# Kernel optimization log

Measured on AMD Instinct MI355X. Metric: run time of the kernel, lower is better.

## Reference

```python
import jax, jax.numpy as jnp
import numpy as np

FEAT_STRIDE = 16
ANCHOR_SCALES = (8.0, 16.0, 32.0)
ANCHOR_RATIOS = (0.5, 1.0, 2.0)
PRE_NMS_TOPN = 12000
POST_NMS_TOPN = 2000
NMS_THRESH = 0.7
MIN_SIZE = 16.0


def _mkanchors(ws, hs, cx, cy):
    return np.stack([cx - 0.5 * (ws - 1), cy - 0.5 * (hs - 1),
                     cx + 0.5 * (ws - 1), cy + 0.5 * (hs - 1)], axis=1)


def generate_anchors(base_size=16, ratios=ANCHOR_RATIOS, scales=ANCHOR_SCALES):
    ratios = np.asarray(ratios, np.float32)
    scales = np.asarray(scales, np.float32)
    w = h = float(base_size)
    cx = cy = 0.5 * (base_size - 1)
    size = w * h
    ws = np.round(np.sqrt(size / ratios))
    hs = np.round(ws * ratios)
    ratio_anchors = _mkanchors(ws, hs, cx, cy)
    out = []
    for a in ratio_anchors:
        aw = a[2] - a[0] + 1.0
        ah = a[3] - a[1] + 1.0
        acx = a[0] + 0.5 * (aw - 1)
        acy = a[1] + 0.5 * (ah - 1)
        out.append(_mkanchors(aw * scales, ah * scales, acx, acy))
    return np.concatenate(out, axis=0).astype(np.float32)  # (A, 4)


ANCHORS = generate_anchors(FEAT_STRIDE)
NUM_ANCHORS = ANCHORS.shape[0]  # 9


def _proposal_forward(scores, bbox_deltas, im_info):
    A = NUM_ANCHORS
    fg = scores[:, A:, :, :]                       # (1, A, H, W) foreground scores
    H, W = fg.shape[-2], fg.shape[-1]
    im_h, im_w, im_scale = im_info[0, 0], im_info[0, 1], im_info[0, 2]

    # anchor grid
    sx = jnp.arange(W, dtype=jnp.float32) * FEAT_STRIDE
    sy = jnp.arange(H, dtype=jnp.float32) * FEAT_STRIDE
    gy, gx = jnp.meshgrid(sy, sx, indexing='ij')
    shifts = jnp.stack([gx.ravel(), gy.ravel(), gx.ravel(), gy.ravel()], axis=1)  # (K,4)
    anchors = jnp.asarray(ANCHORS)[None, :, :] + shifts[:, None, :]
    anchors = anchors.reshape(-1, 4)               # (K*A, 4)

    deltas = jnp.transpose(bbox_deltas, (0, 2, 3, 1)).reshape(-1, 4)
    sc = jnp.transpose(fg, (0, 2, 3, 1)).reshape(-1)

    # bbox_transform_inv
    aw = anchors[:, 2] - anchors[:, 0] + 1.0
    ah = anchors[:, 3] - anchors[:, 1] + 1.0
    acx = anchors[:, 0] + 0.5 * aw
    acy = anchors[:, 1] + 0.5 * ah
    pcx = deltas[:, 0] * aw + acx
    pcy = deltas[:, 1] * ah + acy
    pw = jnp.exp(deltas[:, 2]) * aw
    ph = jnp.exp(deltas[:, 3]) * ah
    x1 = pcx - 0.5 * pw
    y1 = pcy - 0.5 * ph
    x2 = pcx + 0.5 * pw
    y2 = pcy + 0.5 * ph

    # clip_boxes (scale slot in the clip call is 1.0 in the original)
    x1 = jnp.clip(x1, 0.0, im_w - 1.0)
    x2 = jnp.clip(x2, 0.0, im_w - 1.0)
    y1 = jnp.clip(y1, 0.0, im_h - 1.0)
    y2 = jnp.clip(y2, 0.0, im_h - 1.0)
    props = jnp.stack([x1, y1, x2, y2], axis=1)

    # _filter_boxes: mask instead of gather (jit-safe fixed shapes)
    ms = MIN_SIZE * im_scale
    valid = ((x2 - x1 + 1.0) >= ms) & ((y2 - y1 + 1.0) >= ms)
    sc_m = jnp.where(valid, sc, -jnp.inf)

    # descending sort + pre-NMS top-k in one shot
    top_sc, order = jax.lax.top_k(sc_m, PRE_NMS_TOPN)
    p = props[order]                               # (preN, 4) sorted by score desc
    vk = valid[order]

    pn = jax.lax.stop_gradient(p)
    areas = (pn[:, 2] - pn[:, 0] + 1.0) * (pn[:, 3] - pn[:, 1] + 1.0)
    xx1 = jnp.maximum(pn[:, 0][:, None], pn[:, 0][None, :])
    yy1 = jnp.maximum(pn[:, 1][:, None], pn[:, 1][None, :])
    xx2 = jnp.minimum(pn[:, 2][:, None], pn[:, 2][None, :])
    yy2 = jnp.minimum(pn[:, 3][:, None], pn[:, 3][None, :])
    inter = jnp.maximum(xx2 - xx1 + 1.0, 0.0) * jnp.maximum(yy2 - yy1 + 1.0, 0.0)
    iou = inter / (areas[:, None] + areas[None, :] - inter)
    sup_mat = iou > NMS_THRESH                     # (preN, preN) bool

    idx = jnp.arange(PRE_NMS_TOPN, dtype=jnp.int32)

    def body(keep, xs):
        sup_row, i = xs
        keep = jnp.where(keep[i], keep & ~(sup_row & (idx > i)), keep)
        return keep, None

    keep, _ = jax.lax.scan(body, vk, (sup_mat, idx))

    # keep[:post_nms_topN] with fixed shapes: rank kept boxes, scatter into slots
    rank = jnp.cumsum(keep.astype(jnp.int32)) - 1
    slot_src = jnp.where(keep & (rank < POST_NMS_TOPN), rank, POST_NMS_TOPN)
    slots = jnp.full((POST_NMS_TOPN,), PRE_NMS_TOPN, jnp.int32).at[slot_src].set(idx, mode='drop')

    p_pad = jnp.concatenate([p, jnp.zeros((1, 4), p.dtype)], axis=0)
    s_pad = jnp.concatenate([top_sc, jnp.zeros((1,), top_sc.dtype)], axis=0)
    boxes = p_pad[slots]
    out_sc = s_pad[slots][:, None]
    rois = jnp.concatenate([jnp.zeros((POST_NMS_TOPN, 1), boxes.dtype), boxes], axis=1)
    return rois, out_sc


def setup_inputs() -> dict:
    key = jax.random.key(0)
    k1, k2 = jax.random.split(key)
    H = W = 512
    scores = jax.random.normal(k1, (1, 2 * NUM_ANCHORS, H, W), jnp.float32)
    bbox_deltas = jax.random.normal(k2, (1, 4 * NUM_ANCHORS, H, W), jnp.float32) * 0.2
    im_info = jnp.array([[float(H * FEAT_STRIDE), float(W * FEAT_STRIDE), 1.0]], jnp.float32)
    return {"scores": scores, "bbox_deltas": bbox_deltas, "im_info": im_info}


def reference(scores, bbox_deltas, im_info):
    return _proposal_forward(scores, bbox_deltas, im_info)
```

## Files before the change

### kernel.cpp

```cpp
#include <hip/hip_runtime.h>
#include <hip/hip_bf16.h>
#include <stdint.h>

#pragma clang fp contract(off)

#define FH 512
#define FW 512
#define NA 9
#define HW (FH*FW)
#define TOTAL (HW*NA)
#define PRE_NMS 12000
#define POST_NMS 2000
#define NMS_WORDS 188
#define MROW 192
#define CAND_MAX 16384
#define NMS_TH 0.7f
#define MIN_SIZE_C 16.0f

__constant__ float ANCH[NA][4] = {
  {-84.f,-40.f,99.f,55.f},
  {-176.f,-88.f,191.f,103.f},
  {-360.f,-184.f,375.f,199.f},
  {-56.f,-56.f,71.f,71.f},
  {-120.f,-120.f,135.f,135.f},
  {-248.f,-248.f,263.f,263.f},
  {-36.f,-80.f,51.f,95.f},
  {-80.f,-168.f,95.f,183.f},
  {-168.f,-344.f,183.f,359.f}
};

__device__ __forceinline__ void decode_box(int a, int h, int w,
    const float* __restrict__ deltas, float im_h, float im_w,
    float& x1, float& y1, float& x2, float& y2) {
  float sx = (float)(w * 16);
  float sy = (float)(h * 16);
  float ax1 = ANCH[a][0] + sx;
  float ay1 = ANCH[a][1] + sy;
  float ax2 = ANCH[a][2] + sx;
  float ay2 = ANCH[a][3] + sy;
  float aw = ax2 - ax1 + 1.0f;
  float ah = ay2 - ay1 + 1.0f;
  float acx = ax1 + 0.5f * aw;
  float acy = ay1 + 0.5f * ah;
  int base = h * FW + w;
  float d0 = deltas[(4*a+0)*HW + base];
  float d1 = deltas[(4*a+1)*HW + base];
  float d2 = deltas[(4*a+2)*HW + base];
  float d3 = deltas[(4*a+3)*HW + base];
  float pcx = d0 * aw + acx;
  float pcy = d1 * ah + acy;
  float pw = expf(d2) * aw;
  float ph = expf(d3) * ah;
  x1 = pcx - 0.5f * pw;
  y1 = pcy - 0.5f * ph;
  x2 = pcx + 0.5f * pw;
  y2 = pcy + 0.5f * ph;
  x1 = fminf(fmaxf(x1, 0.0f), im_w - 1.0f);
  x2 = fminf(fmaxf(x2, 0.0f), im_w - 1.0f);
  y1 = fminf(fmaxf(y1, 0.0f), im_h - 1.0f);
  y2 = fminf(fmaxf(y2, 0.0f), im_h - 1.0f);
}

__global__ void k_keys(const float* __restrict__ scores, const float* __restrict__ deltas,
                       const float* __restrict__ im_info, unsigned* __restrict__ keys,
                       unsigned* __restrict__ hist8) {
  __shared__ unsigned lh[256];
  int t = threadIdx.x;
  lh[t] = 0;
  __syncthreads();
  int base = blockIdx.x * blockDim.x + t;
  float im_h = im_info[0], im_w = im_info[1];
  float ms = MIN_SIZE_C * im_info[2];
  int h = base / FW, w = base % FW;
  for (int a = 0; a < NA; a++) {
    float x1, y1, x2, y2;
    decode_box(a, h, w, deltas, im_h, im_w, x1, y1, x2, y2);
    bool valid = ((x2 - x1 + 1.0f) >= ms) && ((y2 - y1 + 1.0f) >= ms);
    float sc = scores[(NA + a)*HW + base];
    float v = valid ? sc : -INFINITY;
    unsigned u = __float_as_uint(v);
    unsigned mono = (u & 0x80000000u) ? ~u : (u | 0x80000000u);
    keys[base*NA + a] = mono;
    atomicAdd(&lh[mono >> 24], 1u);
  }
  __syncthreads();
  atomicAdd(&hist8[t], lh[t]);
}

__global__ void __launch_bounds__(256) k_refine15(const unsigned* __restrict__ keys,
    const unsigned* __restrict__ hist8, unsigned* __restrict__ hist15) {
  __shared__ unsigned ssum[256];
  __shared__ unsigned sB8;
  int t = threadIdx.x;
  unsigned hv = hist8[t];
  ssum[t] = hv;
  __syncthreads();
  for (int off = 1; off < 256; off <<= 1) {
    unsigned v = ssum[t];
    unsigned add = (t + off < 256) ? ssum[t + off] : 0u;
    __syncthreads();
    ssum[t] = v + add;
    __syncthreads();
  }
  unsigned above = ssum[t] - hv;
  if (above < PRE_NMS && above + hv >= PRE_NMS) sB8 = (unsigned)t;
  __syncthreads();
  unsigned B8 = sB8;
  int stride = gridDim.x * blockDim.x;
  for (int i = blockIdx.x * blockDim.x + t; i < TOTAL; i += stride) {
    unsigned k = keys[i];
    if ((k >> 24) == B8) atomicAdd(&hist15[(k >> 9) & 0x7FFFu], 1u);
  }
}

__global__ void __launch_bounds__(256) k_compact(const unsigned* __restrict__ keys,
    const unsigned* __restrict__ hist8, const unsigned* __restrict__ hist15,
    unsigned* __restrict__ cnt, unsigned long long* __restrict__ cand) {
  __shared__ unsigned ssum[256];
  __shared__ unsigned sB8, sT2, sB15;
  int t = threadIdx.x;
  unsigned hv = hist8[t];
  ssum[t] = hv;
  __syncthreads();
  for (int off = 1; off < 256; off <<= 1) {
    unsigned v = ssum[t];
    unsigned add = (t + off < 256) ? ssum[t + off] : 0u;
    __syncthreads();
    ssum[t] = v + add;
    __syncthreads();
  }
  unsigned above = ssum[t] - hv;
  if (above < PRE_NMS && above + hv >= PRE_NMS) { sB8 = (unsigned)t; sT2 = PRE_NMS - above; }
  __syncthreads();
  unsigned B8 = sB8, T2 = sT2;
  unsigned loc = 0;
  for (int i = 0; i < 128; i++) loc += hist15[t*128 + i];
  __syncthreads();
  ssum[t] = loc;
  __syncthreads();
  for (int off = 1; off < 256; off <<= 1) {
    unsigned v = ssum[t];
    unsigned add = (t + off < 256) ? ssum[t + off] : 0u;
    __syncthreads();
    ssum[t] = v + add;
    __syncthreads();
  }
  unsigned above15 = ssum[t] - loc;
  unsigned acc = above15;
  for (int i = 127; i >= 0; i--) {
    unsigned cb = hist15[t*128 + i];
    acc += cb;
    if (acc >= T2 && acc - cb < T2) sB15 = (unsigned)(t*128 + i);
  }
  __syncthreads();
  unsigned K = (B8 << 24) | (sB15 << 9);
  int stride = gridDim.x * blockDim.x;
  for (int i = blockIdx.x * blockDim.x + t; i < TOTAL; i += stride) {
    unsigned k = keys[i];
    if (k >= K) {
      unsigned pos = atomicAdd(cnt, 1u);
      if (pos < CAND_MAX)
        cand[pos] = ((unsigned long long)k << 32) | (unsigned)(~(unsigned)i);
    }
  }
}

__global__ void __launch_bounds__(256) k_rank(const unsigned* __restrict__ pcnt,
    const unsigned long long* __restrict__ cand,
    const float* __restrict__ deltas, const float* __restrict__ im_info,
    float4* __restrict__ boxes, float* __restrict__ scoresArr,
    unsigned long long* __restrict__ remvInit) {
  __shared__ unsigned long long tile[2048];
  unsigned cnt = *pcnt;
  if (cnt > CAND_MAX) cnt = CAND_MAX;
  int i = blockIdx.x * 256 + threadIdx.x;
  unsigned long long mine = (i < (int)cnt) ? cand[i] : 0ULL;
  int rank = 0;
  for (unsigned t0 = 0; t0 < cnt; t0 += 2048) {
    unsigned n = min(2048u, cnt - t0);
    __syncthreads();
    for (unsigned j = threadIdx.x; j < n; j += 256) tile[j] = cand[t0 + j];
    __syncthreads();
    if (i < (int)cnt) {
      int q0 = 0, q1 = 0, q2 = 0, q3 = 0;
      unsigned j = 0;
      #pragma unroll 4
      for (; j + 4 <= n; j += 4) {
        q0 += (tile[j]   > mine) ? 1 : 0;
        q1 += (tile[j+1] > mine) ? 1 : 0;
        q2 += (tile[j+2] > mine) ? 1 : 0;
        q3 += (tile[j+3] > mine) ? 1 : 0;
      }
      for (; j < n; j++) q0 += (tile[j] > mine) ? 1 : 0;
      rank += q0 + q1 + q2 + q3;
    }
  }
  if (i < (int)cnt && rank < PRE_NMS) {
    unsigned mono = (unsigned)(mine >> 32);
    unsigned idx = ~(unsigned)(mine & 0xFFFFFFFFull);
    unsigned u = (mono & 0x80000000u) ? (mono ^ 0x80000000u) : ~mono;
    float sc = __uint_as_float(u);
    int a = idx % NA;
    int base = idx / NA;
    int h = base / FW, w = base % FW;
    float x1, y1, x2, y2;
    decode_box(a, h, w, deltas, im_info[0], im_info[1], x1, y1, x2, y2);
    boxes[rank] = make_float4(x1, y1, x2, y2);
    scoresArr[rank] = sc;
    if (sc > -INFINITY)
      atomicAnd(&remvInit[rank >> 6], ~(1ULL << (rank & 63)));
  }
}

__global__ void __launch_bounds__(64) k_mask(const float4* __restrict__ boxes,
                                             unsigned long long* __restrict__ mask) {
  int wg = blockIdx.x;
  int bi = blockIdx.y;
  if (wg * 8 + 7 < bi) return;
  __shared__ float4 jb[8][64];
  int t = threadIdx.x;
  #pragma unroll
  for (int k = 0; k < 8; k++) {
    int jg = (wg * 8 + k) * 64 + t;
    jb[k][t] = (jg < PRE_NMS) ? boxes[jg] : make_float4(0.f, 0.f, -1.f, -1.f);
  }
  __syncthreads();
  int i = bi * 64 + t;
  if (i >= PRE_NMS) return;
  float4 b = boxes[i];
  float area_i = (b.z - b.x + 1.0f) * (b.w - b.y + 1.0f);
  unsigned long long bits[8];
  #pragma unroll
  for (int k = 0; k < 8; k++) {
    unsigned long long bb = 0;
    for (int jj = 0; jj < 64; jj++) {
      float4 o = jb[k][jj];
      float xx1 = fmaxf(b.x, o.x);
      float yy1 = fmaxf(b.y, o.y);
      float xx2 = fminf(b.z, o.z);
      float yy2 = fminf(b.w, o.w);
      float iw = fmaxf(xx2 - xx1 + 1.0f, 0.0f);
      float ih = fmaxf(yy2 - yy1 + 1.0f, 0.0f);
      float inter = iw * ih;
      float area_o = (o.z - o.x + 1.0f) * (o.w - o.y + 1.0f);
      float iou = inter / (area_i + area_o - inter);
      if (iou > NMS_TH) bb |= (1ULL << jj);
    }
    bits[k] = bb;
  }
  size_t rb = (size_t)i * MROW + wg * 8;
  #pragma unroll
  for (int k = 0; k < 8; k++) mask[rb + k] = bits[k];
}

__global__ void __launch_bounds__(64) k_nms(const unsigned long long* __restrict__ mask,
    const unsigned long long* __restrict__ remvI,
    const float4* __restrict__ boxes, const float* __restrict__ scoresArr,
    float* __restrict__ out) {
  extern __shared__ unsigned long long dyn[];
  unsigned long long* stage = dyn;
  unsigned* klist = (unsigned*)(dyn + 64 * MROW);
  int lane = threadIdx.x;
  unsigned long long r0 = remvI[lane];
  unsigned long long r1 = remvI[64 + lane];
  unsigned long long r2 = remvI[128 + lane];
  unsigned long long W = __shfl(r0, 0);
  unsigned long long diagc = mask[(size_t)lane * MROW + 0];
  unsigned long long nw1c  = mask[(size_t)lane * MROW + 1];
  int kept_cnt = 0, nkPrev = 0;
  bool done = false;
  for (int c = 0; c < NMS_WORDS; c++) {
    bool more = (c + 1 < NMS_WORDS);
    unsigned long long diagN = 0, nw1N = 0;
    if (more) {
      size_t rb = (size_t)((c + 1) * 64 + lane) * MROW;
      diagN = mask[rb + (c + 1)];
      if (c + 2 < NMS_WORDS) nw1N = mask[rb + (c + 2)];
    }
    int gi0 = c * 64;
    int jmax = PRE_NMS - gi0; if (jmax > 64) jmax = 64;
    unsigned long long avail = ~W;
    if (jmax < 64) avail &= ((1ULL << jmax) - 1ULL);
    unsigned long long keptmask = 0;
    while (avail) {
      int j = __ffsll((long long)avail) - 1;
      keptmask |= (1ULL << j);
      if (lane == 0) klist[kept_cnt] = (unsigned)(gi0 + j);
      kept_cnt++;
      if (kept_cnt >= POST_NMS) { done = true; break; }
      unsigned long long supp = __shfl(diagc, j);
      avail &= ~supp;
      avail &= ~((2ULL << j) - 1ULL);
    }
    if (done || !more) break;
    unsigned long long A = ((keptmask >> lane) & 1ULL) ? nw1c : 0ULL;
    asm volatile("s_waitcnt vmcnt(0)" ::: "memory");
    __builtin_amdgcn_sched_barrier(0);
    for (int s = 0; s < nkPrev; s++) {
      r0 |= stage[s * MROW + lane];
      r1 |= stage[s * MROW + 64 + lane];
      r2 |= stage[s * MROW + 128 + lane];
    }
    unsigned long long x = A;
    #pragma unroll
    for (int off = 32; off; off >>= 1) x |= __shfl_xor(x, off);
    int cw = c + 1;
    unsigned long long Rw = ((cw >> 6) == 0) ? r0 : (((cw >> 6) == 1) ? r1 : r2);
    W = __shfl(Rw, cw & 63) | x;
    int slot = 0;
    unsigned long long km = keptmask;
    while (km) {
      int j = __ffsll((long long)km) - 1; km &= km - 1;
      const char* rb = (const char*)(mask + (size_t)(gi0 + j) * MROW);
      char* lb = (char*)(void*)stage + slot * 1536;
      __builtin_amdgcn_global_load_lds(
          (const __attribute__((address_space(1))) unsigned*)(rb + lane * 16),
          (__attribute__((address_space(3))) unsigned*)lb, 16, 0, 0);
      if (lane < 30)
        __builtin_amdgcn_global_load_lds(
            (const __attribute__((address_space(1))) unsigned*)(rb + 1024 + lane * 16),
            (__attribute__((address_space(3))) unsigned*)(lb + 1024), 16, 0, 0);
      slot++;
    }
    nkPrev = slot;
    diagc = diagN; nw1c = nw1N;
  }
  __syncthreads();
  for (int s = lane; s < POST_NMS; s += 64) {
    float x1 = 0.f, y1 = 0.f, x2 = 0.f, y2 = 0.f, sc = 0.f;
    if (s < kept_cnt) {
      unsigned r = klist[s];
      float4 b = boxes[r];
      x1 = b.x; y1 = b.y; x2 = b.z; y2 = b.w;
      sc = scoresArr[r];
    }
    out[s*5 + 0] = 0.f;
    out[s*5 + 1] = x1;
    out[s*5 + 2] = y1;
    out[s*5 + 3] = x2;
    out[s*5 + 4] = y2;
    out[POST_NMS*5 + s] = sc;
  }
}

extern "C" void kernel_launch(void* const* d_in, const int* in_sizes, int n_in,
                              void* d_out, int out_size, void* d_ws, size_t ws_size,
                              hipStream_t stream) {
  const float* scores  = (const float*)d_in[0];
  const float* deltas  = (const float*)d_in[1];
  const float* im_info = (const float*)d_in[2];
  float* out = (float*)d_out;
  char* ws = (char*)d_ws;

  unsigned* keys             = (unsigned*)(ws + 0);
  unsigned* hist8            = (unsigned*)(ws + 9437184);
  unsigned* hist15           = (unsigned*)(ws + 9438208);
  unsigned* scal             = (unsigned*)(ws + 9569280);
  unsigned long long* remvI  = (unsigned long long*)(ws + 9569536);
  unsigned long long* cand   = (unsigned long long*)(ws + 9571072);
  float4* boxes              = (float4*)(ws + 9702144);
  float* scoresArr           = (float*)(ws + 9894144);
  unsigned long long* mask   = (unsigned long long*)(ws + 9942144);

  hipMemsetAsync(ws + 9437184, 0, 132352, stream);
  hipMemsetAsync(ws + 9569536, 0xFF, 1536, stream);

  k_keys<<<HW/256, 256, 0, stream>>>(scores, deltas, im_info, keys, hist8);
  k_refine15<<<256, 256, 0, stream>>>(keys, hist8, hist15);
  k_compact<<<256, 256, 0, stream>>>(keys, hist8, hist15, &scal[4], cand);
  k_rank<<<CAND_MAX/256, 256, 0, stream>>>(&scal[4], cand, deltas, im_info,
                                           boxes, scoresArr, remvI);
  dim3 mg(24, 188);
  k_mask<<<mg, 64, 0, stream>>>(boxes, mask);

  (void)hipFuncSetAttribute((const void*)k_nms,
        hipFuncAttributeMaxDynamicSharedMemorySize, 64*MROW*8 + 2000*4);
  k_nms<<<1, 64, 64*MROW*8 + 2000*4, stream>>>(mask, remvI, boxes, scoresArr, out);
}
```

Measured before the change: 1.012 ms.

## Fuse proposal stages into one cooperative kernel and tighten NMS scan

Replaces the two memsets and five separate kernels (keys, refine, compact, rank, mask) with one cooperative persistent kernel that uses grid syncs between phases. The key layout becomes anchor-major for coalesced stores, and ranking is split across 8 blocks per candidate group with atomic partial sums. In the NMS kernel, shuffles become readlanes, suppression words are accumulated inside the keep loop, and mask rows are prefetched two chunks ahead. This removes launch and memset overhead at the cost of grid-wide barriers and fixed 512-block residency requirements.

```diff
diff --git a/kernel.cpp b/kernel.cpp
--- a/kernel.cpp
+++ b/kernel.cpp
@@ -1,8 +1,10 @@
 #include <hip/hip_runtime.h>
-#include <hip/hip_bf16.h>
+#include <hip/hip_cooperative_groups.h>
 #include <stdint.h>
 
 #pragma clang fp contract(off)
+
+typedef unsigned long long u64;
 
 #define FH 512
 #define FW 512
@@ -13,9 +15,13 @@
 #define POST_NMS 2000
 #define NMS_WORDS 188
 #define MROW 192
+#define MROWS_ALLOC 12032
 #define CAND_MAX 16384
 #define NMS_TH 0.7f
 #define MIN_SIZE_C 16.0f
+#define NBLK 512
+#define NTHR 256
+#define GSIZE (NBLK*NTHR)
 
 __constant__ float ANCH[NA][4] = {
   {-84.f,-40.f,99.f,55.f},
@@ -61,254 +67,275 @@
   y2 = fminf(fmaxf(y2, 0.0f), im_h - 1.0f);
 }
 
-__global__ void k_keys(const float* __restrict__ scores, const float* __restrict__ deltas,
-                       const float* __restrict__ im_info, unsigned* __restrict__ keys,
-                       unsigned* __restrict__ hist8) {
-  __shared__ unsigned lh[256];
-  int t = threadIdx.x;
-  lh[t] = 0;
-  __syncthreads();
-  int base = blockIdx.x * blockDim.x + t;
-  float im_h = im_info[0], im_w = im_info[1];
-  float ms = MIN_SIZE_C * im_info[2];
-  int h = base / FW, w = base % FW;
-  for (int a = 0; a < NA; a++) {
-    float x1, y1, x2, y2;
-    decode_box(a, h, w, deltas, im_h, im_w, x1, y1, x2, y2);
-    bool valid = ((x2 - x1 + 1.0f) >= ms) && ((y2 - y1 + 1.0f) >= ms);
-    float sc = scores[(NA + a)*HW + base];
-    float v = valid ? sc : -INFINITY;
-    unsigned u = __float_as_uint(v);
-    unsigned mono = (u & 0x80000000u) ? ~u : (u | 0x80000000u);
-    keys[base*NA + a] = mono;
-    atomicAdd(&lh[mono >> 24], 1u);
-  }
-  __syncthreads();
-  atomicAdd(&hist8[t], lh[t]);
+__device__ __forceinline__ u64 rl64(u64 v, int l) {
+  unsigned lo = (unsigned)__builtin_amdgcn_readlane((int)(unsigned)(v & 0xFFFFFFFFull), l);
+  unsigned hi = (unsigned)__builtin_amdgcn_readlane((int)(unsigned)(v >> 32), l);
+  return ((u64)hi << 32) | lo;
 }
 
-__global__ void __launch_bounds__(256) k_refine15(const unsigned* __restrict__ keys,
-    const unsigned* __restrict__ hist8, unsigned* __restrict__ hist15) {
-  __shared__ unsigned ssum[256];
-  __shared__ unsigned sB8;
-  int t = threadIdx.x;
-  unsigned hv = hist8[t];
-  ssum[t] = hv;
-  __syncthreads();
-  for (int off = 1; off < 256; off <<= 1) {
-    unsigned v = ssum[t];
-    unsigned add = (t + off < 256) ? ssum[t + off] : 0u;
-    __syncthreads();
-    ssum[t] = v + add;
-    __syncthreads();
-  }
-  unsigned above = ssum[t] - hv;
-  if (above < PRE_NMS && above + hv >= PRE_NMS) sB8 = (unsigned)t;
-  __syncthreads();
-  unsigned B8 = sB8;
-  int stride = gridDim.x * blockDim.x;
-  for (int i = blockIdx.x * blockDim.x + t; i < TOTAL; i += stride) {
-    unsigned k = keys[i];
-    if ((k >> 24) == B8) atomicAdd(&hist15[(k >> 9) & 0x7FFFu], 1u);
+__global__ void __launch_bounds__(NTHR, 2) k_mega(
+    const float* __restrict__ scores, const float* __restrict__ deltas,
+    const float* __restrict__ im_info, unsigned* __restrict__ keys,
+    unsigned* __restrict__ hist8, unsigned* __restrict__ hist15,
+    unsigned* __restrict__ scal, u64* __restrict__ remvI,
+    u64* __restrict__ cand, unsigned* __restrict__ rankArr,
+    float4* __restrict__ boxes, float* __restrict__ scoresArr,
+    u64* __restrict__ mask) {
+  cooperative_groups::grid_group gg = cooperative_groups::this_grid();
+  __shared__ u64 smem[2048];
+  __shared__ unsigned svar[4];
+  unsigned* sh32 = (unsigned*)smem;
+  int t = threadIdx.x, b = blockIdx.x;
+  int gtid = b * NTHR + t;
+
+  if (gtid < 256)       hist8[gtid] = 0;
+  if (gtid < 32768)     hist15[gtid] = 0;
+  if (gtid < 64)        scal[gtid] = 0;
+  if (gtid < 192)       remvI[gtid] = ~0ULL;
+  if (gtid < CAND_MAX)  rankArr[gtid] = 0;
+  gg.sync();
+
+  {
+    sh32[t] = 0;
+    __syncthreads();
+    float im_h = im_info[0], im_w = im_info[1];
+    float ms = MIN_SIZE_C * im_info[2];
+    for (int rep = 0; rep < 2; rep++) {
+      int base = gtid + rep * GSIZE;
+      int h = base >> 9, w = base & 511;
+      for (int a = 0; a < NA; a++) {
+        float x1, y1, x2, y2;
+        decode_box(a, h, w, deltas, im_h, im_w, x1, y1, x2, y2);
+        bool valid = ((x2 - x1 + 1.0f) >= ms) && ((y2 - y1 + 1.0f) >= ms);
+        float sc = scores[(NA + a)*HW + base];
+        float v = valid ? sc : -INFINITY;
+        unsigned u = __float_as_uint(v);
+        unsigned mono = (u & 0x80000000u) ? ~u : (u | 0x80000000u);
+        keys[a*HW + base] = mono;
+        atomicAdd(&sh32[mono >> 24], 1u);
+      }
+    }
+    __syncthreads();
+    atomicAdd(&hist8[t], sh32[t]);
+  }
+  gg.sync();
+
+  {
+    unsigned hv = hist8[t];
+    sh32[t] = hv;
+    __syncthreads();
+    for (int off = 1; off < 256; off <<= 1) {
+      unsigned v = sh32[t];
+      unsigned add = (t + off < 256) ? sh32[t + off] : 0u;
+      __syncthreads();
+      sh32[t] = v + add;
+      __syncthreads();
+    }
+    unsigned above = sh32[t] - hv;
+    if (above < PRE_NMS && above + hv >= PRE_NMS) svar[0] = (unsigned)t;
+    __syncthreads();
+    unsigned B8 = svar[0];
+    for (int i = gtid; i < TOTAL; i += GSIZE) {
+      unsigned k = keys[i];
+      if ((k >> 24) == B8) atomicAdd(&hist15[(k >> 9) & 0x7FFFu], 1u);
+    }
+  }
+  gg.sync();
+
+  {
+    unsigned hv = hist8[t];
+    __syncthreads();
+    sh32[t] = hv;
+    __syncthreads();
+    for (int off = 1; off < 256; off <<= 1) {
+      unsigned v = sh32[t];
+      unsigned add = (t + off < 256) ? sh32[t + off] : 0u;
+      __syncthreads();
+      sh32[t] = v + add;
+      __syncthreads();
+    }
+    unsigned above = sh32[t] - hv;
+    if (above < PRE_NMS && above + hv >= PRE_NMS) { svar[0] = (unsigned)t; svar[1] = PRE_NMS - above; }
+    __syncthreads();
+    unsigned B8 = svar[0], T2 = svar[1];
+    unsigned loc = 0;
+    for (int i = 0; i < 128; i++) loc += hist15[t*128 + i];
+    __syncthreads();
+    sh32[t] = loc;
+    __syncthreads();
+    for (int off = 1; off < 256; off <<= 1) {
+      unsigned v = sh32[t];
+      unsigned add = (t + off < 256) ? sh32[t + off] : 0u;
+      __syncthreads();
+      sh32[t] = v + add;
+      __syncthreads();
+    }
+    unsigned above15 = sh32[t] - loc;
+    unsigned acc = above15;
+    for (int i = 127; i >= 0; i--) {
+      unsigned cb = hist15[t*128 + i];
+      acc += cb;
+      if (acc >= T2 && acc - cb < T2) svar[2] = (unsigned)(t*128 + i);
+    }
+    __syncthreads();
+    unsigned K = (B8 << 24) | (svar[2] << 9);
+    for (int i = gtid; i < TOTAL; i += GSIZE) {
+      unsigned k = keys[i];
+      if (k >= K) {
+        unsigned pos = atomicAdd(&scal[4], 1u);
+        if (pos < CAND_MAX) {
+          unsigned a = ((unsigned)i) >> 18;
+          unsigned base2 = ((unsigned)i) & 262143u;
+          unsigned oi = base2 * 9u + a;
+          cand[pos] = ((u64)k << 32) | (unsigned)(~oi);
+        }
+      }
+    }
+  }
+  gg.sync();
+
+  {
+    unsigned cnt = scal[4]; if (cnt > CAND_MAX) cnt = CAND_MAX;
+    int ig = b >> 3, oc = b & 7;
+    unsigned jn = (cnt + 7) >> 3;
+    unsigned j0 = oc * jn;
+    unsigned j1 = j0 + jn; if (j1 > cnt) j1 = cnt;
+    if (j0 > cnt) j0 = cnt;
+    for (unsigned j = j0 + t; j < j1; j += NTHR) smem[j - j0] = cand[j];
+    __syncthreads();
+    int i = ig * NTHR + t;
+    if (i < (int)cnt && j1 > j0) {
+      u64 mine = cand[i];
+      int n = (int)(j1 - j0);
+      int q0 = 0, q1 = 0, q2 = 0, q3 = 0, j = 0;
+      for (; j + 4 <= n; j += 4) {
+        q0 += (smem[j]   > mine) ? 1 : 0;
+        q1 += (smem[j+1] > mine) ? 1 : 0;
+        q2 += (smem[j+2] > mine) ? 1 : 0;
+        q3 += (smem[j+3] > mine) ? 1 : 0;
+      }
+      for (; j < n; j++) q0 += (smem[j] > mine) ? 1 : 0;
+      int part = q0 + q1 + q2 + q3;
+      if (part) atomicAdd(&rankArr[i], (unsigned)part);
+    }
+  }
+  gg.sync();
+
+  {
+    unsigned cnt = scal[4]; if (cnt > CAND_MAX) cnt = CAND_MAX;
+    if (gtid < (int)cnt) {
+      u64 mine = cand[gtid];
+      unsigned rank = rankArr[gtid];
+      if (rank < PRE_NMS) {
+        unsigned mono = (unsigned)(mine >> 32);
+        unsigned idx = ~(unsigned)(mine & 0xFFFFFFFFull);
+        unsigned u = (mono & 0x80000000u) ? (mono ^ 0x80000000u) : ~mono;
+        float sc = __uint_as_float(u);
+        int a = idx % NA;
+        int base = idx / NA;
+        int h = base / FW, w = base % FW;
+        float x1, y1, x2, y2;
+        decode_box(a, h, w, deltas, im_info[0], im_info[1], x1, y1, x2, y2);
+        boxes[rank] = make_float4(x1, y1, x2, y2);
+        scoresArr[rank] = sc;
+        if (sc > -INFINITY)
+          atomicAnd(&remvI[rank >> 6], ~(1ULL << (rank & 63)));
+      }
+    }
+  }
+  gg.sync();
+
+  {
+    float4* jb = (float4*)smem;
+    for (int u = b; u < 24 * 47; u += NBLK) {
+      int wg = u % 24;
+      int bg = u / 24;
+      if (wg * 8 + 7 < bg * 4) continue;
+      __syncthreads();
+      for (int q = t; q < 512; q += NTHR) {
+        int jg = wg * 512 + q;
+        jb[q] = (jg < PRE_NMS) ? boxes[jg] : make_float4(0.f, 0.f, -1.f, -1.f);
+      }
+      __syncthreads();
+      int i = bg * 256 + t;
+      if (i < PRE_NMS && wg * 8 + 7 >= (i >> 6)) {
+        float4 bx = boxes[i];
+        float area_i = (bx.z - bx.x + 1.0f) * (bx.w - bx.y + 1.0f);
+        u64 bits[8];
+        #pragma unroll
+        for (int k = 0; k < 8; k++) {
+          u64 bb = 0;
+          for (int jj = 0; jj < 64; jj++) {
+            float4 o = jb[k * 64 + jj];
+            float xx1 = fmaxf(bx.x, o.x);
+            float yy1 = fmaxf(bx.y, o.y);
+            float xx2 = fminf(bx.z, o.z);
+            float yy2 = fminf(bx.w, o.w);
+            float iw = fmaxf(xx2 - xx1 + 1.0f, 0.0f);
+            float ih = fmaxf(yy2 - yy1 + 1.0f, 0.0f);
+            float inter = iw * ih;
+            float area_o = (o.z - o.x + 1.0f) * (o.w - o.y + 1.0f);
+            float iou = inter / (area_i + area_o - inter);
+            if (iou > NMS_TH) bb |= (1ULL << jj);
+          }
+          bits[k] = bb;
+        }
+        size_t rb = (size_t)i * MROW + wg * 8;
+        #pragma unroll
+        for (int k = 0; k < 8; k++) mask[rb + k] = bits[k];
+      }
+    }
   }
 }
 
-__global__ void __launch_bounds__(256) k_compact(const unsigned* __restrict__ keys,
-    const unsigned* __restrict__ hist8, const unsigned* __restrict__ hist15,
-    unsigned* __restrict__ cnt, unsigned long long* __restrict__ cand) {
-  __shared__ unsigned ssum[256];
-  __shared__ unsigned sB8, sT2, sB15;
-  int t = threadIdx.x;
-  unsigned hv = hist8[t];
-  ssum[t] = hv;
-  __syncthreads();
-  for (int off = 1; off < 256; off <<= 1) {
-    unsigned v = ssum[t];
-    unsigned add = (t + off < 256) ? ssum[t + off] : 0u;
-    __syncthreads();
-    ssum[t] = v + add;
-    __syncthreads();
-  }
-  unsigned above = ssum[t] - hv;
-  if (above < PRE_NMS && above + hv >= PRE_NMS) { sB8 = (unsigned)t; sT2 = PRE_NMS - above; }
-  __syncthreads();
-  unsigned B8 = sB8, T2 = sT2;
-  unsigned loc = 0;
-  for (int i = 0; i < 128; i++) loc += hist15[t*128 + i];
-  __syncthreads();
-  ssum[t] = loc;
-  __syncthreads();
-  for (int off = 1; off < 256; off <<= 1) {
-    unsigned v = ssum[t];
-    unsigned add = (t + off < 256) ? ssum[t + off] : 0u;
-    __syncthreads();
-    ssum[t] = v + add;
-    __syncthreads();
-  }
-  unsigned above15 = ssum[t] - loc;
-  unsigned acc = above15;
-  for (int i = 127; i >= 0; i--) {
-    unsigned cb = hist15[t*128 + i];
-    acc += cb;
-    if (acc >= T2 && acc - cb < T2) sB15 = (unsigned)(t*128 + i);
-  }
-  __syncthreads();
-  unsigned K = (B8 << 24) | (sB15 << 9);
-  int stride = gridDim.x * blockDim.x;
-  for (int i = blockIdx.x * blockDim.x + t; i < TOTAL; i += stride) {
-    unsigned k = keys[i];
-    if (k >= K) {
-      unsigned pos = atomicAdd(cnt, 1u);
-      if (pos < CAND_MAX)
-        cand[pos] = ((unsigned long long)k << 32) | (unsigned)(~(unsigned)i);
-    }
-  }
-}
-
-__global__ void __launch_bounds__(256) k_rank(const unsigned* __restrict__ pcnt,
-    const unsigned long long* __restrict__ cand,
-    const float* __restrict__ deltas, const float* __restrict__ im_info,
-    float4* __restrict__ boxes, float* __restrict__ scoresArr,
-    unsigned long long* __restrict__ remvInit) {
-  __shared__ unsigned long long tile[2048];
-  unsigned cnt = *pcnt;
-  if (cnt > CAND_MAX) cnt = CAND_MAX;
-  int i = blockIdx.x * 256 + threadIdx.x;
-  unsigned long long mine = (i < (int)cnt) ? cand[i] : 0ULL;
-  int rank = 0;
-  for (unsigned t0 = 0; t0 < cnt; t0 += 2048) {
-    unsigned n = min(2048u, cnt - t0);
-    __syncthreads();
-    for (unsigned j = threadIdx.x; j < n; j += 256) tile[j] = cand[t0 + j];
-    __syncthreads();
-    if (i < (int)cnt) {
-      int q0 = 0, q1 = 0, q2 = 0, q3 = 0;
-      unsigned j = 0;
-      #pragma unroll 4
-      for (; j + 4 <= n; j += 4) {
-        q0 += (tile[j]   > mine) ? 1 : 0;
-        q1 += (tile[j+1] > mine) ? 1 : 0;
-        q2 += (tile[j+2] > mine) ? 1 : 0;
-        q3 += (tile[j+3] > mine) ? 1 : 0;
-      }
-      for (; j < n; j++) q0 += (tile[j] > mine) ? 1 : 0;
-      rank += q0 + q1 + q2 + q3;
-    }
-  }
-  if (i < (int)cnt && rank < PRE_NMS) {
-    unsigned mono = (unsigned)(mine >> 32);
-    unsigned idx = ~(unsigned)(mine & 0xFFFFFFFFull);
-    unsigned u = (mono & 0x80000000u) ? (mono ^ 0x80000000u) : ~mono;
-    float sc = __uint_as_float(u);
-    int a = idx % NA;
-    int base = idx / NA;
-    int h = base / FW, w = base % FW;
-    float x1, y1, x2, y2;
-    decode_box(a, h, w, deltas, im_info[0], im_info[1], x1, y1, x2, y2);
-    boxes[rank] = make_float4(x1, y1, x2, y2);
-    scoresArr[rank] = sc;
-    if (sc > -INFINITY)
-      atomicAnd(&remvInit[rank >> 6], ~(1ULL << (rank & 63)));
-  }
-}
-
-__global__ void __launch_bounds__(64) k_mask(const float4* __restrict__ boxes,
-                                             unsigned long long* __restrict__ mask) {
-  int wg = blockIdx.x;
-  int bi = blockIdx.y;
-  if (wg * 8 + 7 < bi) return;
-  __shared__ float4 jb[8][64];
-  int t = threadIdx.x;
-  #pragma unroll
-  for (int k = 0; k < 8; k++) {
-    int jg = (wg * 8 + k) * 64 + t;
-    jb[k][t] = (jg < PRE_NMS) ? boxes[jg] : make_float4(0.f, 0.f, -1.f, -1.f);
-  }
-  __syncthreads();
-  int i = bi * 64 + t;
-  if (i >= PRE_NMS) return;
-  float4 b = boxes[i];
-  float area_i = (b.z - b.x + 1.0f) * (b.w - b.y + 1.0f);
-  unsigned long long bits[8];
-  #pragma unroll
-  for (int k = 0; k < 8; k++) {
-    unsigned long long bb = 0;
-    for (int jj = 0; jj < 64; jj++) {
-      float4 o = jb[k][jj];
-      float xx1 = fmaxf(b.x, o.x);
-      float yy1 = fmaxf(b.y, o.y);
-      float xx2 = fminf(b.z, o.z);
-      float yy2 = fminf(b.w, o.w);
-      float iw = fmaxf(xx2 - xx1 + 1.0f, 0.0f);
-      float ih = fmaxf(yy2 - yy1 + 1.0f, 0.0f);
-      float inter = iw * ih;
-      float area_o = (o.z - o.x + 1.0f) * (o.w - o.y + 1.0f);
-      float iou = inter / (area_i + area_o - inter);
-      if (iou > NMS_TH) bb |= (1ULL << jj);
-    }
-    bits[k] = bb;
-  }
-  size_t rb = (size_t)i * MROW + wg * 8;
-  #pragma unroll
-  for (int k = 0; k < 8; k++) mask[rb + k] = bits[k];
-}
-
-__global__ void __launch_bounds__(64) k_nms(const unsigned long long* __restrict__ mask,
-    const unsigned long long* __restrict__ remvI,
+__global__ void __launch_bounds__(64) k_nms(const u64* __restrict__ mask,
+    const u64* __restrict__ remvI,
     const float4* __restrict__ boxes, const float* __restrict__ scoresArr,
     float* __restrict__ out) {
-  extern __shared__ unsigned long long dyn[];
-  unsigned long long* stage = dyn;
+  extern __shared__ u64 dyn[];
+  u64* stage = dyn;
   unsigned* klist = (unsigned*)(dyn + 64 * MROW);
   int lane = threadIdx.x;
-  unsigned long long r0 = remvI[lane];
-  unsigned long long r1 = remvI[64 + lane];
-  unsigned long long r2 = remvI[128 + lane];
-  unsigned long long W = __shfl(r0, 0);
-  unsigned long long diagc = mask[(size_t)lane * MROW + 0];
-  unsigned long long nw1c  = mask[(size_t)lane * MROW + 1];
+  u64 r0 = remvI[lane];
+  u64 r1 = remvI[64 + lane];
+  u64 r2 = remvI[128 + lane];
+  u64 W = rl64(r0, 0);
+  u64 diagc = mask[(size_t)lane * MROW + 0];
+  u64 nw1c  = mask[(size_t)lane * MROW + 1];
+  u64 diagn = mask[(size_t)(64 + lane) * MROW + 1];
+  u64 nw1n  = mask[(size_t)(64 + lane) * MROW + 2];
   int kept_cnt = 0, nkPrev = 0;
   bool done = false;
   for (int c = 0; c < NMS_WORDS; c++) {
-    bool more = (c + 1 < NMS_WORDS);
-    unsigned long long diagN = 0, nw1N = 0;
-    if (more) {
-      size_t rb = (size_t)((c + 1) * 64 + lane) * MROW;
-      diagN = mask[rb + (c + 1)];
-      if (c + 2 < NMS_WORDS) nw1N = mask[rb + (c + 2)];
-    }
     int gi0 = c * 64;
     int jmax = PRE_NMS - gi0; if (jmax > 64) jmax = 64;
-    unsigned long long avail = ~W;
+    u64 avail = ~W;
     if (jmax < 64) avail &= ((1ULL << jmax) - 1ULL);
-    unsigned long long keptmask = 0;
+    u64 keptmask = 0, A = 0;
     while (avail) {
       int j = __ffsll((long long)avail) - 1;
       keptmask |= (1ULL << j);
       if (lane == 0) klist[kept_cnt] = (unsigned)(gi0 + j);
       kept_cnt++;
       if (kept_cnt >= POST_NMS) { done = true; break; }
-      unsigned long long supp = __shfl(diagc, j);
+      u64 supp = rl64(diagc, j);
+      A |= rl64(nw1c, j);
       avail &= ~supp;
       avail &= ~((2ULL << j) - 1ULL);
     }
-    if (done || !more) break;
-    unsigned long long A = ((keptmask >> lane) & 1ULL) ? nw1c : 0ULL;
+    if (done || c + 1 >= NMS_WORDS) break;
     asm volatile("s_waitcnt vmcnt(0)" ::: "memory");
     __builtin_amdgcn_sched_barrier(0);
     for (int s = 0; s < nkPrev; s++) {
-      r0 |= stage[s * MROW + lane];
-      r1 |= stage[s * MROW + 64 + lane];
-      r2 |= stage[s * MROW + 128 + lane];
-    }
-    unsigned long long x = A;
-    #pragma unroll
-    for (int off = 32; off; off >>= 1) x |= __shfl_xor(x, off);
+      r0 |= stage[(size_t)s * MROW + lane];
+      r1 |= stage[(size_t)s * MROW + 64 + lane];
+      r2 |= stage[(size_t)s * MROW + 128 + lane];
+    }
     int cw = c + 1;
-    unsigned long long Rw = ((cw >> 6) == 0) ? r0 : (((cw >> 6) == 1) ? r1 : r2);
-    W = __shfl(Rw, cw & 63) | x;
+    u64 Rw = (cw < 64) ? r0 : ((cw < 128) ? r1 : r2);
+    W = rl64(Rw, cw & 63) | A;
     int slot = 0;
-    unsigned long long km = keptmask;
+    u64 km = keptmask;
     while (km) {
       int j = __ffsll((long long)km) - 1; km &= km - 1;
       const char* rb = (const char*)(mask + (size_t)(gi0 + j) * MROW);
@@ -316,14 +343,20 @@
       __builtin_amdgcn_global_load_lds(
           (const __attribute__((address_space(1))) unsigned*)(rb + lane * 16),
           (__attribute__((address_space(3))) unsigned*)lb, 16, 0, 0);
-      if (lane < 30)
+      if (lane < 32)
         __builtin_amdgcn_global_load_lds(
             (const __attribute__((address_space(1))) unsigned*)(rb + 1024 + lane * 16),
             (__attribute__((address_space(3))) unsigned*)(lb + 1024), 16, 0, 0);
       slot++;
     }
     nkPrev = slot;
-    diagc = diagN; nw1c = nw1N;
+    u64 d2 = 0, n2 = 0;
+    if (c + 2 < NMS_WORDS) {
+      size_t rb = (size_t)((c + 2) * 64 + lane) * MROW;
+      d2 = mask[rb + (c + 2)];
+      if (c + 3 < NMS_WORDS) n2 = mask[rb + (c + 3)];
+    }
+    diagc = diagn; nw1c = nw1n; diagn = d2; nw1n = n2;
   }
   __syncthreads();
   for (int s = lane; s < POST_NMS; s += 64) {
@@ -352,28 +385,24 @@
   float* out = (float*)d_out;
   char* ws = (char*)d_ws;
 
-  unsigned* keys             = (unsigned*)(ws + 0);
-  unsigned* hist8            = (unsigned*)(ws + 9437184);
-  unsigned* hist15           = (unsigned*)(ws + 9438208);
-  unsigned* scal             = (unsigned*)(ws + 9569280);
-  unsigned long long* remvI  = (unsigned long long*)(ws + 9569536);
-  unsigned long long* cand   = (unsigned long long*)(ws + 9571072);
-  float4* boxes              = (float4*)(ws + 9702144);
-  float* scoresArr           = (float*)(ws + 9894144);
-  unsigned long long* mask   = (unsigned long long*)(ws + 9942144);
-
-  hipMemsetAsync(ws + 9437184, 0, 132352, stream);
-  hipMemsetAsync(ws + 9569536, 0xFF, 1536, stream);
-
-  k_keys<<<HW/256, 256, 0, stream>>>(scores, deltas, im_info, keys, hist8);
-  k_refine15<<<256, 256, 0, stream>>>(keys, hist8, hist15);
-  k_compact<<<256, 256, 0, stream>>>(keys, hist8, hist15, &scal[4], cand);
-  k_rank<<<CAND_MAX/256, 256, 0, stream>>>(&scal[4], cand, deltas, im_info,
-                                           boxes, scoresArr, remvI);
-  dim3 mg(24, 188);
-  k_mask<<<mg, 64, 0, stream>>>(boxes, mask);
+  unsigned* keys    = (unsigned*)(ws + 0);
+  unsigned* hist8   = (unsigned*)(ws + 9437184);
+  unsigned* hist15  = (unsigned*)(ws + 9438208);
+  unsigned* scal    = (unsigned*)(ws + 9569280);
+  u64* remvI        = (u64*)(ws + 9569536);
+  u64* cand         = (u64*)(ws + 9571072);
+  unsigned* rankArr = (unsigned*)(ws + 9702144);
+  float4* boxes     = (float4*)(ws + 9767680);
+  float* scoresArr  = (float*)(ws + 9960192);
+  u64* mask         = (u64*)(ws + 10008576);
+
+  void* args[] = { (void*)&scores, (void*)&deltas, (void*)&im_info, (void*)&keys,
+                   (void*)&hist8, (void*)&hist15, (void*)&scal, (void*)&remvI,
+                   (void*)&cand, (void*)&rankArr, (void*)&boxes, (void*)&scoresArr,
+                   (void*)&mask };
+  hipLaunchCooperativeKernel((void*)k_mega, dim3(NBLK), dim3(NTHR), args, 0, stream);
 
   (void)hipFuncSetAttribute((const void*)k_nms,
-        hipFuncAttributeMaxDynamicSharedMemorySize, 64*MROW*8 + 2000*4);
-  k_nms<<<1, 64, 64*MROW*8 + 2000*4, stream>>>(mask, remvI, boxes, scoresArr, out);
+        hipFuncAttributeMaxDynamicSharedMemorySize, 64*MROW*8 + POST_NMS*4);
+  k_nms<<<1, 64, 64*MROW*8 + POST_NMS*4, stream>>>(mask, remvI, boxes, scoresArr, out);
 }
```

Measured after the change: 1.064 ms. +5.2%, slower.
